# Optimization experiments

Measured on AMD Instinct MI355X. Metric: run time of the kernel, lower is better.

The kernel has to match this reference:

```python
import jax, jax.numpy as jnp
import numpy as np

T, B, D = 256, 256, 512
H, DK = 8, 64          # num_heads, d_kv; inner_dim = H*DK = 512
NUM_GROUPS = 16


def setup_inputs() -> dict:
    key = jax.random.key(0)
    ks = jax.random.split(key, 6)
    hidden_states = jax.random.normal(ks[0], (T, B, D), dtype=jnp.float32)
    # sorted group ids over the batch axis (what _infer_group_ids_from_mask recovers)
    group_ids = jnp.sort(jax.random.randint(ks[1], (B,), 0, NUM_GROUPS, dtype=jnp.int32))
    scale = 1.0 / np.sqrt(D)
    Wq = jax.random.normal(ks[2], (D, H * DK), dtype=jnp.float32) * scale
    Wk = jax.random.normal(ks[3], (D, H * DK), dtype=jnp.float32) * scale
    Wv = jax.random.normal(ks[4], (D, H * DK), dtype=jnp.float32) * scale
    Wo = jax.random.normal(ks[5], (H * DK, D), dtype=jnp.float32) * scale
    return {"hidden_states": hidden_states, "group_ids": group_ids,
            "Wq": Wq, "Wk": Wk, "Wv": Wv, "Wo": Wo}


def reference(hidden_states, group_ids, Wq, Wk, Wv, Wo):
    # Group-restricted self-attention along the batch axis, per time step & head.
    # Equivalent to the block-sparse MiniFlash kernel: entries attend only to
    # batch entries with the same group id.
    t, b, d = hidden_states.shape
    q = (hidden_states @ Wq).reshape(t, b, H, DK)
    k = (hidden_states @ Wk).reshape(t, b, H, DK)
    v = (hidden_states @ Wv).reshape(t, b, H, DK)
    sm_scale = 1.0 / np.sqrt(DK)
    # scores: [T, H, B, B] over the batch axis
    scores = jnp.einsum("tihd,tjhd->thij", q, k) * sm_scale
    allowed = group_ids[:, None] == group_ids[None, :]          # [B, B]
    neg = jnp.finfo(scores.dtype).min
    scores = jnp.where(allowed[None, None, :, :], scores, neg)
    attn = jax.nn.softmax(scores, axis=-1)
    out = jnp.einsum("thij,tjhd->tihd", attn, v).reshape(t, b, H * DK)
    return out @ Wo
```

## Files before the change

kernel.cpp:

```cpp
#include <hip/hip_runtime.h>
#include <hip/hip_bf16.h>

typedef __attribute__((ext_vector_type(8))) short short8;
typedef __attribute__((ext_vector_type(4))) short short4v;
typedef __attribute__((ext_vector_type(4))) float f32x4;

#define MFMA16(a, b, c) __builtin_amdgcn_mfma_f32_16x16x32_bf16(a, b, c, 0, 0, 0)

__device__ __forceinline__ unsigned short f2bf(float f) {
    union { __hip_bfloat16 h; unsigned short u; } v;
    v.h = __float2bfloat16(f);
    return v.u;
}

__device__ __forceinline__ short8 pack8(float4 a, float4 b) {
    short8 p;
    p[0] = (short)f2bf(a.x); p[1] = (short)f2bf(a.y);
    p[2] = (short)f2bf(a.z); p[3] = (short)f2bf(a.w);
    p[4] = (short)f2bf(b.x); p[5] = (short)f2bf(b.y);
    p[6] = (short)f2bf(b.z); p[7] = (short)f2bf(b.w);
    return p;
}

__device__ __forceinline__ int swz64(int row, int bytecol) {
    return row * 64 + ((bytecol ^ ((row & 7) << 4)) >> 1);
}
__device__ __forceinline__ int swz256(int row, int bytecol) {
    return row * 256 + ((bytecol ^ ((row & 7) << 4)) >> 1);
}
__device__ __forceinline__ int swz32(int row, int bytecol) {
    return row * 32 + ((bytecol ^ ((row & 3) << 4)) >> 1);
}

__device__ __forceinline__ void async16(void* lds_uniform, const void* gsrc) {
    __builtin_amdgcn_global_load_lds(
        (const __attribute__((address_space(1))) unsigned int*)gsrc,
        (__attribute__((address_space(3))) unsigned int*)lds_uniform,
        16, 0, 0);
}

__global__ __launch_bounds__(256) void wprep(
    const float* __restrict__ Wq, const float* __restrict__ Wk,
    const float* __restrict__ Wv, const float* __restrict__ Wo,
    unsigned short* __restrict__ wt, int swz)
{
    __shared__ float tile[64][65];
    const int bid = blockIdx.x;
    const int m = bid >> 6, tb = bid & 63;
    const int kr = (tb >> 3) << 6, nc = (tb & 7) << 6;
    const float* W = (m == 0) ? Wq : (m == 1) ? Wk : (m == 2) ? Wv : Wo;
    const int tid = threadIdx.x;
    for (int i = tid; i < 4096; i += 256)
        tile[i >> 6][i & 63] = W[(size_t)(kr + (i >> 6)) * 512 + nc + (i & 63)];
    __syncthreads();
    unsigned short* dst = wt + (size_t)m * 262144;
    for (int i = tid; i < 4096; i += 256) {
        const int n = nc + (i >> 6);
        const int e = i & 63;
        const int rsw = swz ? ((n & 7) * 8) : 0;
        dst[(size_t)n * 512 + kr + e] = f2bf(tile[e ^ rsw][i >> 6]);
    }
}

__global__ __launch_bounds__(256) void xprep(
    const float* __restrict__ hs, unsigned short* __restrict__ xb)
{
    const long long total = 4194304;
    for (long long g = (long long)blockIdx.x * 256 + threadIdx.x; g < total;
         g += (long long)gridDim.x * 256) {
        const int row = (int)(g >> 6);
        const int e0  = ((int)g & 63) * 8;
        const int src = e0 ^ ((row & 7) * 8);
        const float* s = hs + (size_t)row * 512 + src;
        const float4 f0 = *(const float4*)s;
        const float4 f1 = *(const float4*)(s + 4);
        *(short8*)(xb + (size_t)row * 512 + e0) = pack8(f0, f1);
    }
}

template<int F32OUT>
__global__ __launch_bounds__(256) void gemm_glds(
    const unsigned short* __restrict__ A,
    const unsigned short* __restrict__ B,
    unsigned short* __restrict__ obf,
    float* __restrict__ of32,
    int nbcnt)
{
    __shared__ unsigned short As[128 * 64];
    __shared__ unsigned short Bs[128 * 64];

    const int orig  = blockIdx.x;
    const int chunk = gridDim.x >> 3;
    const int wg = (orig & 7) * chunk + (orig >> 3);
    const int mb = wg / nbcnt;
    const int nb = wg - mb * nbcnt;

    const int tid  = threadIdx.x;
    const int lane = tid & 63;
    const int w    = tid >> 6;
    const int l15  = lane & 15;
    const int hi4  = lane >> 4;
    const int wr   = w >> 1, wc = w & 1;

    f32x4 acc[4][4];
    #pragma unroll
    for (int mt = 0; mt < 4; ++mt)
        #pragma unroll
        for (int nt = 0; nt < 4; ++nt)
            acc[mt][nt] = (f32x4){0.f, 0.f, 0.f, 0.f};

    const char* __restrict__ Ab = (const char*)(A + (size_t)mb * 128 * 512);
    const char* __restrict__ Bb = (const char*)(B + (size_t)nb * 128 * 512);
    const int sbase = w * 4096;

    for (int kb = 0; kb < 512; kb += 64) {
        #pragma unroll
        for (int i = 0; i < 4; ++i) {
            const int sb = sbase + i * 1024;
            const int s  = sb + lane * 16;
            const int row = s >> 7, colb = s & 127;
            const size_t goff = (size_t)row * 1024 + (size_t)kb * 2 + colb;
            async16(&As[sb >> 1], Ab + goff);
            async16(&Bs[sb >> 1], Bb + goff);
        }
        __syncthreads();
        #pragma unroll
        for (int ks = 0; ks < 2; ++ks) {
            short8 af[4];
            #pragma unroll
            for (int mt = 0; mt < 4; ++mt)
                af[mt] = *(const short8*)&As[swz64(wr * 64 + mt * 16 + l15,
                                                   ks * 64 + hi4 * 16)];
            __builtin_amdgcn_s_setprio(1);
            #pragma unroll
            for (int nt = 0; nt < 4; ++nt) {
                const short8 bf = *(const short8*)&Bs[swz64(wc * 64 + nt * 16 + l15,
                                                            ks * 64 + hi4 * 16)];
                #pragma unroll
                for (int mt = 0; mt < 4; ++mt)
                    acc[mt][nt] = MFMA16(af[mt], bf, acc[mt][nt]);
            }
            __builtin_amdgcn_s_setprio(0);
        }
        __syncthreads();
    }

    #pragma unroll
    for (int mt = 0; mt < 4; ++mt) {
        #pragma unroll
        for (int nt = 0; nt < 4; ++nt) {
            const int colt = nb * 128 + wc * 64 + nt * 16 + l15;
            #pragma unroll
            for (int r = 0; r < 4; ++r) {
                const int row = mb * 128 + wr * 64 + mt * 16 + hi4 * 4 + r;
                if (F32OUT) {
                    of32[(size_t)row * 512 + colt] = acc[mt][nt][r];
                } else {
                    const int mat = colt >> 9, cc = colt & 511;
                    obf[(size_t)mat * 33554432 + (size_t)row * 512 + cc] =
                        f2bf(acc[mt][nt][r]);
                }
            }
        }
    }
}

__global__ __launch_bounds__(512, 4) void attn_split(
    unsigned short* __restrict__ qkvb,
    const int* __restrict__ gid,
    int doswz)
{
    __shared__ unsigned short Vt[64 * 256];
    __shared__ unsigned short Ps[256 * 32];

    const int th = blockIdx.x;
    const int t = th >> 3, h = th & 7;
    const int tid  = threadIdx.x;
    const int lane = tid & 63;
    const int w    = tid >> 6;
    const int l15  = lane & 15;
    const int hi4  = lane >> 4;
    const int wrow = w << 5;

    const size_t rowbase = (size_t)t * 256 * 512 + h * 64;
    unsigned short* __restrict__ qb = qkvb + rowbase;
    const unsigned short* __restrict__ kbp = qkvb + 33554432ull + rowbase;
    const unsigned short* __restrict__ vbp = qkvb + 67108864ull + rowbase;

    {
        const int d2 = (tid & 31) * 2;
        const int jg = tid >> 5;
        unsigned int vv[16];
        #pragma unroll
        for (int jj = 0; jj < 16; ++jj)
            vv[jj] = *(const unsigned int*)(vbp + (size_t)(jg * 16 + jj) * 512 + d2);
        short8 a0, a1, b0, b1;
        #pragma unroll
        for (int jj = 0; jj < 8; ++jj) {
            a0[jj] = (short)(vv[jj] & 0xFFFFu);
            b0[jj] = (short)(vv[jj] >> 16);
            a1[jj] = (short)(vv[8 + jj] & 0xFFFFu);
            b1[jj] = (short)(vv[8 + jj] >> 16);
        }
        *(short8*)&Vt[swz256(d2,     jg * 32)]      = a0;
        *(short8*)&Vt[swz256(d2,     jg * 32 + 16)] = a1;
        *(short8*)&Vt[swz256(d2 + 1, jg * 32)]      = b0;
        *(short8*)&Vt[swz256(d2 + 1, jg * 32 + 16)] = b1;
    }
    short8 qf[2][2];
    #pragma unroll
    for (int a = 0; a < 2; ++a)
        #pragma unroll
        for (int ks = 0; ks < 2; ++ks)
            qf[a][ks] = *(const short8*)(qb + (size_t)(wrow + a * 16 + l15) * 512 +
                                          ks * 32 + hi4 * 8);

    int rg[2][4];
    #pragma unroll
    for (int a = 0; a < 2; ++a)
        #pragma unroll
        for (int r = 0; r < 4; ++r)
            rg[a][r] = gid[wrow + a * 16 + hi4 * 4 + r];
    const int gfirst = gid[wrow], glast = gid[wrow + 31];
    int lo = 0, hi2 = 256;
    while (lo < hi2) { const int mid = (lo + hi2) >> 1;
        if (gid[mid] < gfirst) lo = mid + 1; else hi2 = mid; }
    const int klo = lo;
    lo = 0; hi2 = 256;
    while (lo < hi2) { const int mid = (lo + hi2) >> 1;
        if (gid[mid] <= glast) lo = mid + 1; else hi2 = mid; }
    const int khi = lo - 1;

    __syncthreads();

    f32x4 o[2][4];
    float mrun[2][4], lrun[2][4];
    #pragma unroll
    for (int a = 0; a < 2; ++a)
        #pragma unroll
        for (int n = 0; n < 4; ++n)
            o[a][n] = (f32x4){0.f, 0.f, 0.f, 0.f};
    #pragma unroll
    for (int a = 0; a < 2; ++a)
        #pragma unroll
        for (int r = 0; r < 4; ++r) { mrun[a][r] = -3.0e38f; lrun[a][r] = 0.f; }

    for (int kc = klo & ~31; kc <= khi; kc += 32) {
        f32x4 sfr[2][2];
        __builtin_amdgcn_s_setprio(1);
        #pragma unroll
        for (int n = 0; n < 2; ++n) {
            const unsigned short* krp = kbp + (size_t)(kc + n * 16 + l15) * 512;
            const short8 kf0 = *(const short8*)(krp + hi4 * 8);
            const short8 kf1 = *(const short8*)(krp + 32 + hi4 * 8);
            #pragma unroll
            for (int a = 0; a < 2; ++a) {
                f32x4 z = (f32x4){0.f, 0.f, 0.f, 0.f};
                z = MFMA16(qf[a][0], kf0, z);
                z = MFMA16(qf[a][1], kf1, z);
                sfr[a][n] = z;
            }
        }
        __builtin_amdgcn_s_setprio(0);
        int cg[2];
        #pragma unroll
        for (int n = 0; n < 2; ++n) cg[n] = gid[kc + n * 16 + l15];

        #pragma unroll
        for (int a = 0; a < 2; ++a) {
            #pragma unroll
            for (int r = 0; r < 4; ++r) {
                const int gr = rg[a][r];
                float sv[2];
                float smax = -3.0e38f;
                #pragma unroll
                for (int n = 0; n < 2; ++n) {
                    float x = sfr[a][n][r] * 0.125f;
                    x = (cg[n] == gr) ? x : -3.0e38f;
                    sv[n] = x;
                    smax = fmaxf(smax, x);
                }
                smax = fmaxf(smax, __shfl_xor(smax, 1));
                smax = fmaxf(smax, __shfl_xor(smax, 2));
                smax = fmaxf(smax, __shfl_xor(smax, 4));
                smax = fmaxf(smax, __shfl_xor(smax, 8));
                const float newm = fmaxf(mrun[a][r], smax);
                const float corr = __expf(mrun[a][r] - newm);
                float ps = 0.f;
                unsigned short pb[2];
                #pragma unroll
                for (int n = 0; n < 2; ++n) {
                    const float p = (sv[n] > -1.0e38f) ? __expf(sv[n] - newm) : 0.f;
                    ps += p;
                    pb[n] = f2bf(p);
                }
                ps += __shfl_xor(ps, 1); ps += __shfl_xor(ps, 2);
                ps += __shfl_xor(ps, 4); ps += __shfl_xor(ps, 8);
                lrun[a][r] = lrun[a][r] * corr + ps;
                mrun[a][r] = newm;
                #pragma unroll
                for (int n = 0; n < 4; ++n) o[a][n][r] *= corr;
                const int prow = wrow + a * 16 + hi4 * 4 + r;
                #pragma unroll
                for (int n = 0; n < 2; ++n)
                    Ps[swz32(prow, (n * 16 + l15) * 2)] = pb[n];
            }
        }

        __builtin_amdgcn_s_setprio(1);
        #pragma unroll
        for (int a = 0; a < 2; ++a) {
            const short8 pa = *(const short8*)&Ps[swz32(wrow + a * 16 + l15, hi4 * 16)];
            #pragma unroll
            for (int n = 0; n < 4; ++n) {
                const short8 vb = *(const short8*)&Vt[swz256(n * 16 + l15,
                                                             (kc + hi4 * 8) * 2)];
                o[a][n] = MFMA16(pa, vb, o[a][n]);
            }
        }
        __builtin_amdgcn_s_setprio(0);
    }

    #pragma unroll
    for (int a = 0; a < 2; ++a) {
        #pragma unroll
        for (int r = 0; r < 4; ++r) {
            const int row = wrow + a * 16 + hi4 * 4 + r;
            const float inv = 1.0f / lrun[a][r];
            const int rsw = doswz ? ((row & 7) * 8) : 0;
            #pragma unroll
            for (int n = 0; n < 4; ++n) {
                const int cc = n * 16 + l15;
                qb[(size_t)row * 512 + (cc ^ rsw)] = f2bf(o[a][n][r] * inv);
            }
        }
    }
}

__global__ __launch_bounds__(1024, 4) void qkv_gemm2(
    const float* __restrict__ hs,
    const unsigned short* __restrict__ wt,
    unsigned short* __restrict__ qkvb)
{
    __shared__ unsigned short As[128 * 64];
    __shared__ unsigned short Bts[512 * 64];

    const int orig = blockIdx.x;
    const int wg = (orig & 7) * 192 + (orig >> 3);
    const int mb = wg / 3;
    const int nb = wg - mb * 3;

    const int tid  = threadIdx.x;
    const int lane = tid & 63;
    const int w    = tid >> 6;
    const int l15  = lane & 15;
    const int hi4  = lane >> 4;
    const int wr   = w >> 3;
    const int wc   = w & 7;

    f32x4 acc[4][4];
    #pragma unroll
    for (int mt = 0; mt < 4; ++mt)
        #pragma unroll
        for (int nt = 0; nt < 4; ++nt)
            acc[mt][nt] = (f32x4){0.f, 0.f, 0.f, 0.f};

    const int ar = tid >> 3, aq = tid & 7;
    const int bc = tid >> 1, bh = tid & 1;
    const float* __restrict__ asrc = hs + ((size_t)mb * 128 + ar) * 512 + aq * 8;
    const unsigned short* __restrict__ bsrc =
        wt + ((size_t)nb * 512 + bc) * 512 + bh * 32;

    float4 a0, a1;
    short8 b8[4];
    a0 = *(const float4*)asrc;
    a1 = *(const float4*)(asrc + 4);
    #pragma unroll
    for (int q = 0; q < 4; ++q) b8[q] = *(const short8*)(bsrc + q * 8);

    for (int kb = 0; kb < 512; kb += 64) {
        *(short8*)&As[swz64(ar, aq * 16)] = pack8(a0, a1);
        #pragma unroll
        for (int q = 0; q < 4; ++q)
            *(short8*)&Bts[swz64(bc, bh * 64 + q * 16)] = b8[q];
        __syncthreads();
        if (kb < 448) {
            const int kn = kb + 64;
            a0 = *(const float4*)(asrc + kn);
            a1 = *(const float4*)(asrc + kn + 4);
            #pragma unroll
            for (int q = 0; q < 4; ++q)
                b8[q] = *(const short8*)(bsrc + kn + q * 8);
        }
        #pragma unroll
        for (int ks = 0; ks < 2; ++ks) {
            short8 af[4];
            #pragma unroll
            for (int mt = 0; mt < 4; ++mt)
                af[mt] = *(const short8*)&As[swz64(wr * 64 + mt * 16 + l15,
                                                   ks * 64 + hi4 * 16)];
            __builtin_amdgcn_s_setprio(1);
            #pragma unroll
            for (int nt = 0; nt < 4; ++nt) {
                const short8 bf = *(const short8*)&Bts[swz64(wc * 64 + nt * 16 + l15,
                                                             ks * 64 + hi4 * 16)];
                #pragma unroll
                for (int mt = 0; mt < 4; ++mt)
                    acc[mt][nt] = MFMA16(af[mt], bf, acc[mt][nt]);
            }
            __builtin_amdgcn_s_setprio(0);
        }
        __syncthreads();
    }

    unsigned short* __restrict__ dst = qkvb + (size_t)nb * 33554432ull;
    #pragma unroll
    for (int mt = 0; mt < 4; ++mt) {
        #pragma unroll
        for (int nt = 0; nt < 4; ++nt) {
            const int col = wc * 64 + nt * 16 + l15;
            #pragma unroll
            for (int r = 0; r < 4; ++r) {
                const int row = mb * 128 + wr * 64 + mt * 16 + hi4 * 4 + r;
                dst[(size_t)row * 512 + col] = f2bf(acc[mt][nt][r]);
            }
        }
    }
}

__global__ __launch_bounds__(1024, 4) void qkv_attn_mfma(
    const float* __restrict__ hs,
    const int*   __restrict__ gid,
    const float* __restrict__ Wq, const float* __restrict__ Wk,
    const float* __restrict__ Wv,
    float*       __restrict__ out)
{
    __shared__ unsigned short Xs[256 * 64];
    __shared__ unsigned short Wsh[192 * 64];
    __shared__ unsigned short Ksh[256 * 64];
    __shared__ unsigned short Vt[64 * 256];
    __shared__ unsigned short XP[256 * 64];
    __shared__ int sgid[256];
    __shared__ int glo[16], ghi[16];

    const int bid = blockIdx.x;
    const int h   = (bid & 63) >> 3;
    const int t   = ((bid >> 6) << 3) + (bid & 7);

    const int tid  = threadIdx.x;
    const int lane = tid & 63;
    const int w    = tid >> 6;
    const int l15  = lane & 15;
    const int hi4  = lane >> 4;
    const int mg   = w & 3;
    const int ng   = w >> 2;

    if (tid < 16) { glo[tid] = 256; ghi[tid] = -1; }
    __syncthreads();
    if (tid < 256) {
        const int g = gid[tid];
        sgid[tid] = g;
        atomicMin(&glo[g], tid);
        atomicMax(&ghi[g], tid);
    }

    const float* __restrict__ Xbase = hs + (size_t)t * (256 * 512);

    const int xr = tid >> 2, xq = tid & 3;
    const bool doW = tid < 768;
    const int wc = tid >> 2;
    const int wq = tid & 3;
    const int wmat = wc >> 6, wcol = wc & 63;
    const float* __restrict__ wfsrc =
        (wmat == 0) ? Wq : (wmat == 1) ? Wk : Wv;

    f32x4 acc[4][3];
    #pragma unroll
    for (int mt = 0; mt < 4; ++mt)
        #pragma unroll
        for (int nt = 0; nt < 3; ++nt)
            acc[mt][nt] = (f32x4){0.f, 0.f, 0.f, 0.f};

    float4 xf[4];
    short8 w8[2];
    {
        const float* s = Xbase + (size_t)xr * 512 + xq * 16;
        xf[0] = *(const float4*)(s + 0);  xf[1] = *(const float4*)(s + 4);
        xf[2] = *(const float4*)(s + 8);  xf[3] = *(const float4*)(s + 12);
        if (doW) {
            #pragma unroll
            for (int b = 0; b < 2; ++b)
                #pragma unroll
                for (int j = 0; j < 8; ++j)
                    w8[b][j] = (short)f2bf(
                        wfsrc[(size_t)(wq * 16 + b * 8 + j) * 512 + h * 64 + wcol]);
        }
    }

    for (int kb = 0; kb < 512; kb += 64) {
        *(short8*)&Xs[swz64(xr, xq * 32 + 0)]  = pack8(xf[0], xf[1]);
        *(short8*)&Xs[swz64(xr, xq * 32 + 16)] = pack8(xf[2], xf[3]);
        if (doW) {
            *(short8*)&Wsh[swz64(wc, wq * 32 + 0)]  = w8[0];
            *(short8*)&Wsh[swz64(wc, wq * 32 + 16)] = w8[1];
        }
        __syncthreads();
        if (kb < 448) {
            const int kn = kb + 64;
            const float* s = Xbase + (size_t)xr * 512 + kn + xq * 16;
            xf[0] = *(const float4*)(s + 0);  xf[1] = *(const float4*)(s + 4);
            xf[2] = *(const float4*)(s + 8);  xf[3] = *(const float4*)(s + 12);
            if (doW) {
                #pragma unroll
                for (int b = 0; b < 2; ++b)
                    #pragma unroll
                    for (int j = 0; j < 8; ++j)
                        w8[b][j] = (short)f2bf(
                            wfsrc[(size_t)(kn + wq * 16 + b * 8 + j) * 512 + h * 64 + wcol]);
            }
        }
        #pragma unroll
        for (int ks = 0; ks < 2; ++ks) {
            short8 af[4];
            #pragma unroll
            for (int mt = 0; mt < 4; ++mt)
                af[mt] = *(const short8*)&Xs[swz64(mg * 64 + mt * 16 + l15,
                                                   ks * 64 + hi4 * 16)];
            __builtin_amdgcn_s_setprio(1);
            #pragma unroll
            for (int nt = 0; nt < 3; ++nt) {
                const short8 bf = *(const short8*)&Wsh[swz64(ng * 48 + nt * 16 + l15,
                                                             ks * 64 + hi4 * 16)];
                #pragma unroll
                for (int mt = 0; mt < 4; ++mt)
                    acc[mt][nt] = MFMA16(af[mt], bf, acc[mt][nt]);
            }
            __builtin_amdgcn_s_setprio(0);
        }
        __syncthreads();
    }

    #pragma unroll
    for (int nt = 0; nt < 3; ++nt) {
        const int c0 = (ng * 3 + nt) * 16;
        const int m  = c0 >> 6;
        const int d0 = c0 & 63;
        #pragma unroll
        for (int mt = 0; mt < 4; ++mt) {
            const int rowb = mg * 64 + mt * 16 + hi4 * 4;
            if (m == 0) {
                #pragma unroll
                for (int r = 0; r < 4; ++r)
                    XP[swz64(rowb + r, (d0 + l15) * 2)] = f2bf(acc[mt][nt][r]);
            } else if (m == 1) {
                #pragma unroll
                for (int r = 0; r < 4; ++r)
                    Ksh[swz64(rowb + r, (d0 + l15) * 2)] = f2bf(acc[mt][nt][r]);
            } else {
                short4v vv;
                #pragma unroll
                for (int r = 0; r < 4; ++r) vv[r] = (short)f2bf(acc[mt][nt][r]);
                *(short4v*)&Vt[swz256(d0 + l15, rowb * 2)] = vv;
            }
        }
    }
    __syncthreads();

    const int wrow = w << 4;
    int rg[4];
    #pragma unroll
    for (int r = 0; r < 4; ++r) rg[r] = sgid[wrow + hi4 * 4 + r];
    const int klo = glo[sgid[wrow]];
    const int khi = ghi[sgid[wrow + 15]];

    short8 qf[2];
    #pragma unroll
    for (int ks = 0; ks < 2; ++ks)
        qf[ks] = *(const short8*)&XP[swz64(wrow + l15, ks * 64 + hi4 * 16)];

    f32x4 o[4];
    float mrun[4], lrun[4];
    #pragma unroll
    for (int n = 0; n < 4; ++n) o[n] = (f32x4){0.f, 0.f, 0.f, 0.f};
    #pragma unroll
    for (int r = 0; r < 4; ++r) { mrun[r] = -3.0e38f; lrun[r] = 0.f; }

    for (int kc = klo & ~63; kc <= khi; kc += 64) {
        f32x4 sfr[4];
        __builtin_amdgcn_s_setprio(1);
        #pragma unroll
        for (int n = 0; n < 4; ++n) {
            const int krow = kc + n * 16 + l15;
            const short8 kf0 = *(const short8*)&Ksh[swz64(krow, hi4 * 16)];
            const short8 kf1 = *(const short8*)&Ksh[swz64(krow, 64 + hi4 * 16)];
            f32x4 z = (f32x4){0.f, 0.f, 0.f, 0.f};
            z = MFMA16(qf[0], kf0, z);
            z = MFMA16(qf[1], kf1, z);
            sfr[n] = z;
        }
        __builtin_amdgcn_s_setprio(0);
        int cg[4];
        #pragma unroll
        for (int n = 0; n < 4; ++n) cg[n] = sgid[kc + n * 16 + l15];

        #pragma unroll
        for (int r = 0; r < 4; ++r) {
            const int gr = rg[r];
            float sv[4];
            float smax = -3.0e38f;
            #pragma unroll
            for (int n = 0; n < 4; ++n) {
                float x = sfr[n][r] * 0.125f;
                x = (cg[n] == gr) ? x : -3.0e38f;
                sv[n] = x;
                smax = fmaxf(smax, x);
            }
            smax = fmaxf(smax, __shfl_xor(smax, 1));
            smax = fmaxf(smax, __shfl_xor(smax, 2));
            smax = fmaxf(smax, __shfl_xor(smax, 4));
            smax = fmaxf(smax, __shfl_xor(smax, 8));
            const float newm = fmaxf(mrun[r], smax);
            const float corr = __expf(mrun[r] - newm);
            float ps = 0.f;
            unsigned short pb[4];
            #pragma unroll
            for (int n = 0; n < 4; ++n) {
                const float p = (sv[n] > -1.0e38f) ? __expf(sv[n] - newm) : 0.f;
                ps += p;
                pb[n] = f2bf(p);
            }
            ps += __shfl_xor(ps, 1); ps += __shfl_xor(ps, 2);
            ps += __shfl_xor(ps, 4); ps += __shfl_xor(ps, 8);
            lrun[r] = lrun[r] * corr + ps;
            mrun[r] = newm;
            #pragma unroll
            for (int n = 0; n < 4; ++n) o[n][r] *= corr;
            const int prow = wrow + hi4 * 4 + r;
            #pragma unroll
            for (int n = 0; n < 4; ++n)
                XP[swz64(prow, (n * 16 + l15) * 2)] = pb[n];
        }

        const short8 pa0 = *(const short8*)&XP[swz64(wrow + l15, hi4 * 16)];
        const short8 pa1 = *(const short8*)&XP[swz64(wrow + l15, 64 + hi4 * 16)];
        __builtin_amdgcn_s_setprio(1);
        #pragma unroll
        for (int n = 0; n < 4; ++n) {
            const short8 vb0 = *(const short8*)&Vt[swz256(n * 16 + l15, (kc + hi4 * 8) * 2)];
            const short8 vb1 = *(const short8*)&Vt[swz256(n * 16 + l15, (kc + 32 + hi4 * 8) * 2)];
            o[n] = MFMA16(pa0, vb0, o[n]);
            o[n] = MFMA16(pa1, vb1, o[n]);
        }
        __builtin_amdgcn_s_setprio(0);
    }

    float* __restrict__ op = out + (size_t)t * (256 * 512) + h * 64;
    #pragma unroll
    for (int r = 0; r < 4; ++r) {
        const int row = wrow + hi4 * 4 + r;
        const float inv = 1.0f / lrun[r];
        #pragma unroll
        for (int n = 0; n < 4; ++n)
            op[(size_t)row * 512 + n * 16 + l15] = o[n][r] * inv;
    }
}

__global__ __launch_bounds__(1024, 4) void oproj_mfma(
    const float* __restrict__ Wo,
    const unsigned short* __restrict__ wot,
    const unsigned short* __restrict__ abuf,
    float* __restrict__ out)
{
    __shared__ unsigned short As[128 * 40];
    __shared__ unsigned short Bts[512 * 40];

    const int tid  = threadIdx.x;
    const int lane = tid & 63;
    const int w    = tid >> 6;
    const int l15  = lane & 15;
    const int hi4  = lane >> 4;
    const int wr   = w >> 2;
    const int wc   = w & 3;
    const size_t r0 = (size_t)blockIdx.x * 128;

    f32x4 acc[2][8];
    #pragma unroll
    for (int m = 0; m < 2; ++m)
        #pragma unroll
        for (int n = 0; n < 8; ++n)
            acc[m][n] = (f32x4){0.f, 0.f, 0.f, 0.f};

    const bool isA = tid < 512;
    const int bn = tid & 511;
    const int ai = bn >> 2, aq = bn & 3;

    float4 af0, af1;
    short8 a8;
    short8 b8[4];

    if (isA) {
        if (abuf) {
            a8 = *(const short8*)(abuf + (r0 + ai) * 512 + aq * 8);
        } else {
            const float* s = out + (r0 + ai) * 512 + aq * 8;
            af0 = *(const float4*)s; af1 = *(const float4*)(s + 4);
        }
    } else {
        if (wot) {
            #pragma unroll
            for (int q = 0; q < 4; ++q)
                b8[q] = *(const short8*)(wot + (size_t)bn * 512 + q * 8);
        } else {
            #pragma unroll
            for (int q = 0; q < 4; ++q)
                #pragma unroll
                for (int j = 0; j < 8; ++j)
                    b8[q][j] = (short)f2bf(Wo[(size_t)(q * 8 + j) * 512 + bn]);
        }
    }

    for (int kb = 0; kb < 512; kb += 32) {
        if (isA) *(short8*)&As[ai * 40 + aq * 8] = abuf ? a8 : pack8(af0, af1);
        else {
            #pragma unroll
            for (int q = 0; q < 4; ++q)
                *(short8*)&Bts[bn * 40 + q * 8] = b8[q];
        }
        __syncthreads();
        if (kb < 480) {
            const int kn = kb + 32;
            if (isA) {
                if (abuf) {
                    a8 = *(const short8*)(abuf + (r0 + ai) * 512 + kn + aq * 8);
                } else {
                    const float* s = out + (r0 + ai) * 512 + kn + aq * 8;
                    af0 = *(const float4*)s; af1 = *(const float4*)(s + 4);
                }
            } else {
                if (wot) {
                    #pragma unroll
                    for (int q = 0; q < 4; ++q)
                        b8[q] = *(const short8*)(wot + (size_t)bn * 512 + kn + q * 8);
                } else {
                    #pragma unroll
                    for (int q = 0; q < 4; ++q)
                        #pragma unroll
                        for (int j = 0; j < 8; ++j)
                            b8[q][j] = (short)f2bf(Wo[(size_t)(kn + q * 8 + j) * 512 + bn]);
                }
            }
        }
        short8 afr[2];
        #pragma unroll
        for (int m = 0; m < 2; ++m)
            afr[m] = *(const short8*)&As[(wr * 32 + m * 16 + l15) * 40 + hi4 * 8];
        __builtin_amdgcn_s_setprio(1);
        #pragma unroll
        for (int n = 0; n < 8; ++n) {
            const short8 bfr = *(const short8*)&Bts[(wc * 128 + n * 16 + l15) * 40 + hi4 * 8];
            #pragma unroll
            for (int m = 0; m < 2; ++m)
                acc[m][n] = MFMA16(afr[m], bfr, acc[m][n]);
        }
        __builtin_amdgcn_s_setprio(0);
        __syncthreads();
    }

    #pragma unroll
    for (int m = 0; m < 2; ++m)
        #pragma unroll
        for (int n = 0; n < 8; ++n)
            #pragma unroll
            for (int r = 0; r < 4; ++r)
                out[(r0 + wr * 32 + m * 16 + hi4 * 4 + r) * 512 + wc * 128 + n * 16 + l15] =
                    acc[m][n][r];
}

extern "C" void kernel_launch(void* const* d_in, const int* in_sizes, int n_in,
                              void* d_out, int out_size, void* d_ws, size_t ws_size,
                              hipStream_t stream) {
    const float* hs  = (const float*)d_in[0];
    const int*   gid = (const int*)  d_in[1];
    const float* Wq  = (const float*)d_in[2];
    const float* Wk  = (const float*)d_in[3];
    const float* Wv  = (const float*)d_in[4];
    const float* Wo  = (const float*)d_in[5];
    float* outp = (float*)d_out;

    const size_t WT_S  = 1048576;
    const size_t XB_S  = 33554432;
    const size_t QKV_S = 100663296;
    unsigned short* wt = (unsigned short*)d_ws;
    unsigned short* wot = wt + (size_t)3 * 262144;

    if (ws_size >= (WT_S + XB_S + QKV_S) * 2) {
        unsigned short* xb   = wt + WT_S;
        unsigned short* qkvb = xb + XB_S;
        wprep<<<256, 256, 0, stream>>>(Wq, Wk, Wv, Wo, wt, 1);
        xprep<<<2048, 256, 0, stream>>>(hs, xb);
        gemm_glds<0><<<6144, 256, 0, stream>>>(xb, wt, qkvb, nullptr, 12);
        attn_split<<<2048, 512, 0, stream>>>(qkvb, gid, 1);
        gemm_glds<1><<<2048, 256, 0, stream>>>(qkvb, wot, nullptr, outp, 4);
    } else if (ws_size >= (WT_S + QKV_S) * 2) {
        unsigned short* qkvb = wt + WT_S;
        wprep<<<256, 256, 0, stream>>>(Wq, Wk, Wv, Wo, wt, 0);
        qkv_gemm2<<<1536, 1024, 0, stream>>>(hs, wt, qkvb);
        attn_split<<<2048, 512, 0, stream>>>(qkvb, gid, 0);
        oproj_mfma<<<512, 1024, 0, stream>>>(Wo, wot, qkvb, outp);
    } else {
        qkv_attn_mfma<<<2048, 1024, 0, stream>>>(hs, gid, Wq, Wk, Wv, outp);
        oproj_mfma<<<512, 1024, 0, stream>>>(Wo, nullptr, nullptr, outp);
    }
}
```

Measured before the change: 346.6 us.

## Enlarge GEMM tiles to 256x256 with multi-buffered async LDS pipeline

Replaces the 128x128 single-buffered GEMM with a 256x256-tile, 512-thread kernel that double-buffers A and triple-buffers B in LDS. Global-to-LDS loads for later k-steps are issued while MFMAs run on the current one, with vmcnt waits and barriers in place of the full syncthreads pairs. The larger tiles raise arithmetic intensity and cut global traffic per output. In exchange the kernel uses 160KB of LDS and more accumulator registers per block, which lowers occupancy and leaves fewer blocks to fill the device.

Measured after the change: 332.4 us. 1.04x faster.

```diff
diff --git a/kernel.cpp b/kernel.cpp
--- a/kernel.cpp
+++ b/kernel.cpp
@@ -79,15 +79,15 @@
 }
 
 template<int F32OUT>
-__global__ __launch_bounds__(256) void gemm_glds(
+__global__ __launch_bounds__(512, 2) void gemm256(
     const unsigned short* __restrict__ A,
     const unsigned short* __restrict__ B,
     unsigned short* __restrict__ obf,
     float* __restrict__ of32,
     int nbcnt)
 {
-    __shared__ unsigned short As[128 * 64];
-    __shared__ unsigned short Bs[128 * 64];
+    __shared__ unsigned short Ash[2][256 * 64];
+    __shared__ unsigned short Bsh[3][256 * 64];
 
     const int orig  = blockIdx.x;
     const int chunk = gridDim.x >> 3;
@@ -100,65 +100,108 @@
     const int w    = tid >> 6;
     const int l15  = lane & 15;
     const int hi4  = lane >> 4;
-    const int wr   = w >> 1, wc = w & 1;
-
-    f32x4 acc[4][4];
-    #pragma unroll
-    for (int mt = 0; mt < 4; ++mt)
-        #pragma unroll
-        for (int nt = 0; nt < 4; ++nt)
-            acc[mt][nt] = (f32x4){0.f, 0.f, 0.f, 0.f};
-
-    const char* __restrict__ Ab = (const char*)(A + (size_t)mb * 128 * 512);
-    const char* __restrict__ Bb = (const char*)(B + (size_t)nb * 128 * 512);
-    const int sbase = w * 4096;
-
-    for (int kb = 0; kb < 512; kb += 64) {
-        #pragma unroll
-        for (int i = 0; i < 4; ++i) {
-            const int sb = sbase + i * 1024;
-            const int s  = sb + lane * 16;
+    const int wr   = w >> 2;
+    const int wc   = w & 3;
+
+    f32x4 acc[8][4];
+    #pragma unroll
+    for (int m = 0; m < 8; ++m)
+        #pragma unroll
+        for (int n = 0; n < 4; ++n)
+            acc[m][n] = (f32x4){0.f, 0.f, 0.f, 0.f};
+
+    const char* __restrict__ Ab = (const char*)(A + (size_t)mb * 256 * 512);
+    const char* __restrict__ Bb = (const char*)(B + (size_t)nb * 256 * 512);
+
+    auto STAGE_A = [&](int buf, int kt, int j2) {
+        #pragma unroll
+        for (int j = 0; j < 2; ++j) {
+            const int c = w * 4 + j2 * 2 + j;
+            const int sbyte = c * 1024;
+            const int s = sbyte + lane * 16;
             const int row = s >> 7, colb = s & 127;
-            const size_t goff = (size_t)row * 1024 + (size_t)kb * 2 + colb;
-            async16(&As[sb >> 1], Ab + goff);
-            async16(&Bs[sb >> 1], Bb + goff);
-        }
-        __syncthreads();
-        #pragma unroll
-        for (int ks = 0; ks < 2; ++ks) {
-            short8 af[4];
-            #pragma unroll
-            for (int mt = 0; mt < 4; ++mt)
-                af[mt] = *(const short8*)&As[swz64(wr * 64 + mt * 16 + l15,
-                                                   ks * 64 + hi4 * 16)];
+            async16((char*)&Ash[buf][0] + sbyte,
+                    Ab + (size_t)row * 1024 + (size_t)kt * 128 + colb);
+        }
+    };
+    auto STAGE_B = [&](int buf, int kt, int j2) {
+        #pragma unroll
+        for (int j = 0; j < 2; ++j) {
+            const int c = w * 4 + j2 * 2 + j;
+            const int sbyte = c * 1024;
+            const int s = sbyte + lane * 16;
+            const int row = s >> 7, colb = s & 127;
+            async16((char*)&Bsh[buf][0] + sbyte,
+                    Bb + (size_t)row * 1024 + (size_t)kt * 128 + colb);
+        }
+    };
+
+    STAGE_A(0, 0, 0); STAGE_A(0, 0, 1);
+    STAGE_B(0, 0, 0); STAGE_B(0, 0, 1);
+    STAGE_B(1, 1, 0); STAGE_B(1, 1, 1);
+    asm volatile("s_waitcnt vmcnt(4)" ::: "memory");
+    __builtin_amdgcn_s_barrier();
+
+    short8 bfr[4][2];
+
+    for (int t = 0; t < 8; ++t) {
+        const int ab = t & 1;
+        const int bb = t % 3;
+        #pragma unroll
+        for (int p = 0; p < 4; ++p) {
+            short8 af[2][2];
+            #pragma unroll
+            for (int mi = 0; mi < 2; ++mi) {
+                const int row = wr * 128 + (p * 2 + mi) * 16 + l15;
+                af[mi][0] = *(const short8*)&Ash[ab][swz64(row, hi4 * 16)];
+                af[mi][1] = *(const short8*)&Ash[ab][swz64(row, 64 + hi4 * 16)];
+            }
+            if (p == 0) {
+                #pragma unroll
+                for (int nt = 0; nt < 4; ++nt) {
+                    const int col = wc * 64 + nt * 16 + l15;
+                    bfr[nt][0] = *(const short8*)&Bsh[bb][swz64(col, hi4 * 16)];
+                    bfr[nt][1] = *(const short8*)&Bsh[bb][swz64(col, 64 + hi4 * 16)];
+                }
+            }
+            if (p < 2) { if (t < 7) STAGE_A(ab ^ 1, t + 1, p); }
+            else       { if (t < 6) STAGE_B((t + 2) % 3, t + 2, p - 2); }
+
+            __builtin_amdgcn_s_barrier();
             __builtin_amdgcn_s_setprio(1);
             #pragma unroll
             for (int nt = 0; nt < 4; ++nt) {
-                const short8 bf = *(const short8*)&Bs[swz64(wc * 64 + nt * 16 + l15,
-                                                            ks * 64 + hi4 * 16)];
-                #pragma unroll
-                for (int mt = 0; mt < 4; ++mt)
-                    acc[mt][nt] = MFMA16(af[mt], bf, acc[mt][nt]);
+                #pragma unroll
+                for (int mi = 0; mi < 2; ++mi) {
+                    const int m = p * 2 + mi;
+                    acc[m][nt] = MFMA16(af[mi][0], bfr[nt][0], acc[m][nt]);
+                    acc[m][nt] = MFMA16(af[mi][1], bfr[nt][1], acc[m][nt]);
+                }
             }
             __builtin_amdgcn_s_setprio(0);
-        }
-        __syncthreads();
-    }
-
-    #pragma unroll
-    for (int mt = 0; mt < 4; ++mt) {
+            if (p < 3) __builtin_amdgcn_s_barrier();
+        }
+        if (t < 7) {
+            if (t < 6) asm volatile("s_waitcnt vmcnt(4)" ::: "memory");
+            else       asm volatile("s_waitcnt vmcnt(0)" ::: "memory");
+            __builtin_amdgcn_s_barrier();
+        }
+    }
+
+    #pragma unroll
+    for (int m = 0; m < 8; ++m) {
         #pragma unroll
         for (int nt = 0; nt < 4; ++nt) {
-            const int colt = nb * 128 + wc * 64 + nt * 16 + l15;
+            const int colt = nb * 256 + wc * 64 + nt * 16 + l15;
             #pragma unroll
             for (int r = 0; r < 4; ++r) {
-                const int row = mb * 128 + wr * 64 + mt * 16 + hi4 * 4 + r;
+                const int row = mb * 256 + wr * 128 + m * 16 + hi4 * 4 + r;
                 if (F32OUT) {
-                    of32[(size_t)row * 512 + colt] = acc[mt][nt][r];
+                    of32[(size_t)row * 512 + colt] = acc[m][nt][r];
                 } else {
                     const int mat = colt >> 9, cc = colt & 511;
                     obf[(size_t)mat * 33554432 + (size_t)row * 512 + cc] =
-                        f2bf(acc[mt][nt][r]);
+                        f2bf(acc[m][nt][r]);
                 }
             }
         }
@@ -798,9 +841,9 @@
         unsigned short* qkvb = xb + XB_S;
         wprep<<<256, 256, 0, stream>>>(Wq, Wk, Wv, Wo, wt, 1);
         xprep<<<2048, 256, 0, stream>>>(hs, xb);
-        gemm_glds<0><<<6144, 256, 0, stream>>>(xb, wt, qkvb, nullptr, 12);
+        gemm256<0><<<1536, 512, 0, stream>>>(xb, wt, qkvb, nullptr, 6);
         attn_split<<<2048, 512, 0, stream>>>(qkvb, gid, 1);
-        gemm_glds<1><<<2048, 256, 0, stream>>>(qkvb, wot, nullptr, outp, 4);
+        gemm256<1><<<512, 512, 0, stream>>>(qkvb, wot, nullptr, outp, 2);
     } else if (ws_size >= (WT_S + QKV_S) * 2) {
         unsigned short* qkvb = wt + WT_S;
         wprep<<<256, 256, 0, stream>>>(Wq, Wk, Wv, Wo, wt, 0);
```
